# Optimization experiments

Hardware: AMD Instinct MI355X
Metric: run time of the kernel (lower is better)

The kernel has to match this reference:

```python
import jax, jax.numpy as jnp
import numpy as np

N = 100000
E = 1600000
D = 128  # in_dim == hidden_dim


def _glorot(key, shape):
    lim = np.sqrt(6.0 / (shape[0] + shape[1]))
    return jax.random.uniform(key, shape, jnp.float32, -lim, lim)


def setup_inputs() -> dict:
    key = jax.random.key(0)
    ks = jax.random.split(key, 10)
    x = jax.random.normal(ks[0], (N, D), jnp.float32)
    edge_index = jax.random.randint(ks[1], (2, E), 0, N, jnp.int64)
    return {
        "x": x,
        "edge_index": edge_index,
        "W1": _glorot(ks[2], (D, D)), "b1": jnp.zeros((D,), jnp.float32),
        "W2": _glorot(ks[3], (D, D)), "b2": jnp.zeros((D,), jnp.float32),
        "Wv": _glorot(ks[4], (D, D)), "bv": jnp.zeros((D,), jnp.float32),
        "Wt": _glorot(ks[5], (D, D)), "bt": jnp.zeros((D,), jnp.float32),
    }


def _gcn_conv(x, W, b, src, dst, dis):
    """GCNConv: x' = D^-1/2 (A+I) D^-1/2 (x W) + b (symmetric norm, self-loops)."""
    xw = x @ W  # [N, H]
    coef = dis[src] * dis[dst]  # [E]
    msg = xw[src] * coef[:, None]  # [E, H] gathered messages
    agg = jax.ops.segment_sum(msg, dst, num_segments=x.shape[0])
    agg = agg + (dis * dis)[:, None] * xw  # self-loop contribution
    return agg + b


def reference(x, edge_index, W1, b1, W2, b2, Wv, bv, Wt, bt):
    src, dst = edge_index[0], edge_index[1]
    n = x.shape[0]
    # degree including self-loop; rsqrt normalization
    deg = jax.ops.segment_sum(jnp.ones_like(dst, dtype=x.dtype), dst, num_segments=n) + 1.0
    dis = jax.lax.rsqrt(deg)
    h = jax.nn.relu(_gcn_conv(x, W1, b1, src, dst, dis))  # dropout: eval no-op
    h = _gcn_conv(h, W2, b2, src, dst, dis)  # last layer: no relu
    x_vision = jax.nn.relu(h @ Wv + bv)
    x_text = jax.nn.relu(h @ Wt + bt)
    return (h, x_vision, x_text)
```

## Files before the change

### kernel.cpp

```cpp
#include <hip/hip_runtime.h>
#include <hip/hip_bf16.h>
#include <hip/hip_fp16.h>

#define NODES 100000
#define EDGES 1600000
#define DIM   128
#define NB    782
#define KA    4096

typedef __bf16   bf16x8 __attribute__((ext_vector_type(8)));
typedef float    f32x4  __attribute__((ext_vector_type(4)));
typedef _Float16 f16x8  __attribute__((ext_vector_type(8)));

__device__ __forceinline__ void gather16(const void* gp, void* lp) {
    __builtin_amdgcn_global_load_lds(
        (const __attribute__((address_space(1))) void*)gp,
        (__attribute__((address_space(3))) void*)lp, 16, 0, 0);
}

__device__ __forceinline__ int wave_detect_m64(const void* ei) {
    const unsigned int* u = (const unsigned int*)ei;
    const unsigned long long nz = __ballot(u[2 * (threadIdx.x & 63) + 1] != 0);
    return (nz == 0ULL) ? 1 : 0;
}

__device__ __forceinline__ int load_idx(const void* ei, long long pos, int m64) {
    return m64 ? (int)((const long long*)ei)[pos] : ((const int*)ei)[pos];
}

__global__ __launch_bounds__(256) void init_kernel(
    int* __restrict__ deg, int zcnt4, int zb,
    const float* __restrict__ Wa, const float* __restrict__ Wb,
    const float* __restrict__ Wc, const float* __restrict__ Wd,
    __bf16* __restrict__ wfout)
{
    const int bid = blockIdx.x;
    if (bid < zb) {
        const int i4 = bid * 256 + threadIdx.x;
        if (i4 < zcnt4) ((int4*)deg)[i4] = make_int4(0, 0, 0, 0);
    } else {
        const int pb = bid - zb;
        const int m  = pb >> 6;
        const int d  = (pb & 63) * 256 + threadIdx.x;
        const float* W = (m == 0) ? Wa : (m == 1) ? Wb : (m == 2) ? Wc : Wd;
        const int j  = d & 7;
        const int l  = (d >> 3) & 15;
        const int q  = (d >> 7) & 3;
        const int kt = (d >> 9) & 3;
        const int ct = (d >> 11) & 7;
        wfout[m * 16384 + d] = (__bf16)W[(kt * 32 + q * 8 + j) * DIM + ct * 16 + l];
    }
}

template <int RELU_BIAS, int ABF16, int OUTF16>
__device__ __forceinline__ void gemm_body(
    const void* __restrict__ Ain, const __bf16* __restrict__ Wf,
    const float* __restrict__ bias, void* __restrict__ outp, int M, int bid)
{
    const int wave = threadIdx.x >> 6;
    const int lane = threadIdx.x & 63;
    const int l15  = lane & 15;
    const int quad = lane >> 4;

    const int row0 = bid * 128 + wave * 32;
    if (row0 >= M) return;

    bf16x8 afA[4], afB[4];
#pragma unroll
    for (int t = 0; t < 2; t++) {
        const int arow  = row0 + t * 16 + l15;
        const int arowc = arow < M ? arow : (M - 1);
        bf16x8* af = t ? afB : afA;
        if (ABF16) {
            const __bf16* ap = (const __bf16*)Ain + (size_t)arowc * DIM + quad * 8;
#pragma unroll
            for (int kt = 0; kt < 4; kt++) af[kt] = *(const bf16x8*)(ap + kt * 32);
        } else {
            const float* ap = (const float*)Ain + (size_t)arowc * DIM + quad * 8;
#pragma unroll
            for (int kt = 0; kt < 4; kt++) {
                const f32x4 lo = *(const f32x4*)(ap + kt * 32);
                const f32x4 hi = *(const f32x4*)(ap + kt * 32 + 4);
                bf16x8 r;
#pragma unroll
                for (int j = 0; j < 4; j++) { r[j] = (__bf16)lo[j]; r[j + 4] = (__bf16)hi[j]; }
                af[kt] = r;
            }
        }
    }

#pragma unroll
    for (int ct = 0; ct < 8; ct++) {
        f32x4 cA = {0.f, 0.f, 0.f, 0.f};
        f32x4 cB = {0.f, 0.f, 0.f, 0.f};
#pragma unroll
        for (int kt = 0; kt < 4; kt++) {
            const bf16x8 b = *(const bf16x8*)(Wf + (ct * 4 + kt) * 512 + lane * 8);
            cA = __builtin_amdgcn_mfma_f32_16x16x32_bf16(afA[kt], b, cA, 0, 0, 0);
            cB = __builtin_amdgcn_mfma_f32_16x16x32_bf16(afB[kt], b, cB, 0, 0, 0);
        }
        const float bb = RELU_BIAS ? bias[ct * 16 + l15] : 0.f;
#pragma unroll
        for (int t = 0; t < 2; t++) {
            const f32x4 c = t ? cB : cA;
#pragma unroll
            for (int r = 0; r < 4; r++) {
                const int row = row0 + t * 16 + quad * 4 + r;
                if (row < M) {
                    float v = c[r];
                    if (RELU_BIAS) { v += bb; v = v > 0.f ? v : 0.f; }
                    const size_t idx = (size_t)row * DIM + ct * 16 + l15;
                    if (OUTF16) ((_Float16*)outp)[idx] = (_Float16)v;
                    else        ((float*)outp)[idx]    = v;
                }
            }
        }
    }
}

template <int RELU_BIAS, int ABF16, int OUTF16>
__global__ __launch_bounds__(256) void gemm128_kernel(
    const void* __restrict__ Ain, const __bf16* __restrict__ Wf,
    const float* __restrict__ bias, void* __restrict__ outp, int M)
{
    gemm_body<RELU_BIAS, ABF16, OUTF16>(Ain, Wf, bias, outp, M, blockIdx.x);
}

__global__ __launch_bounds__(256) void gemm1_count_kernel(
    const float* __restrict__ x, const __bf16* __restrict__ wf1,
    _Float16* __restrict__ xwh, int M, int gm,
    const void* __restrict__ ei, int* __restrict__ deg, int e_cnt)
{
    const int bid = blockIdx.x;
    if (bid < gm) {
        gemm_body<0, 0, 1>(x, wf1, nullptr, xwh, M, bid);
    } else {
        const int m64 = wave_detect_m64(ei);
        const int i = (bid - gm) * 256 + threadIdx.x;
        if (i < e_cnt)
            atomicAdd(&deg[load_idx(ei, (long long)EDGES + i, m64)], 1);
    }
}

__global__ __launch_bounds__(256) void gemm128_dual_kernel(
    const float* __restrict__ A,
    const __bf16* __restrict__ Wf1, const float* __restrict__ b1,
    const __bf16* __restrict__ Wf2, const float* __restrict__ b2,
    float* __restrict__ out1, float* __restrict__ out2, int M)
{
    const int wave = threadIdx.x >> 6;
    const int lane = threadIdx.x & 63;
    const int l15  = lane & 15;
    const int quad = lane >> 4;

    const int row0 = blockIdx.x * 128 + wave * 32;
    if (row0 >= M) return;

    bf16x8 afA[4], afB[4];
#pragma unroll
    for (int t = 0; t < 2; t++) {
        const int arow  = row0 + t * 16 + l15;
        const int arowc = arow < M ? arow : (M - 1);
        const float* ap = A + (size_t)arowc * DIM + quad * 8;
        bf16x8* af = t ? afB : afA;
#pragma unroll
        for (int kt = 0; kt < 4; kt++) {
            const f32x4 lo = *(const f32x4*)(ap + kt * 32);
            const f32x4 hi = *(const f32x4*)(ap + kt * 32 + 4);
            bf16x8 r;
#pragma unroll
            for (int j = 0; j < 4; j++) { r[j] = (__bf16)lo[j]; r[j + 4] = (__bf16)hi[j]; }
            af[kt] = r;
        }
    }

#pragma unroll
    for (int ct = 0; ct < 8; ct++) {
        f32x4 cA1 = {0.f,0.f,0.f,0.f}, cA2 = {0.f,0.f,0.f,0.f};
        f32x4 cB1 = {0.f,0.f,0.f,0.f}, cB2 = {0.f,0.f,0.f,0.f};
#pragma unroll
        for (int kt = 0; kt < 4; kt++) {
            const bf16x8 w1 = *(const bf16x8*)(Wf1 + (ct * 4 + kt) * 512 + lane * 8);
            const bf16x8 w2 = *(const bf16x8*)(Wf2 + (ct * 4 + kt) * 512 + lane * 8);
            cA1 = __builtin_amdgcn_mfma_f32_16x16x32_bf16(afA[kt], w1, cA1, 0, 0, 0);
            cA2 = __builtin_amdgcn_mfma_f32_16x16x32_bf16(afA[kt], w2, cA2, 0, 0, 0);
            cB1 = __builtin_amdgcn_mfma_f32_16x16x32_bf16(afB[kt], w1, cB1, 0, 0, 0);
            cB2 = __builtin_amdgcn_mfma_f32_16x16x32_bf16(afB[kt], w2, cB2, 0, 0, 0);
        }
        const float bb1 = b1[ct * 16 + l15];
        const float bb2 = b2[ct * 16 + l15];
#pragma unroll
        for (int t = 0; t < 2; t++) {
            const f32x4 c1 = t ? cB1 : cA1;
            const f32x4 c2 = t ? cB2 : cA2;
#pragma unroll
            for (int r = 0; r < 4; r++) {
                const int row = row0 + t * 16 + quad * 4 + r;
                if (row < M) {
                    float v1 = c1[r] + bb1; v1 = v1 > 0.f ? v1 : 0.f;
                    float v2 = c2[r] + bb2; v2 = v2 > 0.f ? v2 : 0.f;
                    out1[(size_t)row * DIM + ct * 16 + l15] = v1;
                    out2[(size_t)row * DIM + ct * 16 + l15] = v2;
                }
            }
        }
    }
}

__global__ __launch_bounds__(256) void scan1_kernel(const int* __restrict__ deg,
                                                    int* __restrict__ offs,
                                                    int* __restrict__ bsum,
                                                    float* __restrict__ dis, int n) {
    __shared__ int sm[256];
    const int t = threadIdx.x, i = blockIdx.x * 256 + t;
    const int v = (i < n) ? deg[i] : 0;
    sm[t] = v;
    __syncthreads();
    for (int d = 1; d < 256; d <<= 1) {
        const int add = (t >= d) ? sm[t - d] : 0;
        __syncthreads();
        sm[t] += add;
        __syncthreads();
    }
    if (i < n) {
        offs[i] = sm[t] - v;
        dis[i]  = rsqrtf((float)v + 1.0f);
    }
    if (t == 255) bsum[blockIdx.x] = sm[255];
}

__global__ __launch_bounds__(256) void scan23_kernel(int* __restrict__ offs,
                                                     const int* __restrict__ bsum,
                                                     int* __restrict__ bcur, int n) {
    __shared__ int sm[256];
    const int t = threadIdx.x, bid = blockIdx.x;
    int part = 0;
    for (int j = t; j < bid; j += 256) part += bsum[j];
    sm[t] = part;
    __syncthreads();
    for (int d = 128; d > 0; d >>= 1) {
        if (t < d) sm[t] += sm[t + d];
        __syncthreads();
    }
    const int boff = sm[0];
    const int i = bid * 256 + t;
    if (i < n) {
        const int o = offs[i] + boff;
        offs[i] = o;
        if ((i & 127) == 0) bcur[i >> 7] = o;
    }
    if (bid == 0 && t == 0) offs[n] = EDGES;
}

__global__ __launch_bounds__(256) void bucketA_kernel(
    const void* __restrict__ ei, int* __restrict__ bcur,
    int2* __restrict__ stage, int e_cnt)
{
    __shared__ int2 sstage[KA];
    __shared__ int hist[NB], lofs[NB], lcur[NB], gbase[NB];
    __shared__ int sm[256];
    const int m64 = wave_detect_m64(ei);
    const int t = threadIdx.x;
    const int base = blockIdx.x * KA;
    int cnt = e_cnt - base; cnt = cnt < KA ? cnt : KA;

    for (int i = t; i < NB; i += 256) hist[i] = 0;
    __syncthreads();

    for (int j = t; j < cnt; j += 256) {
        const int d = load_idx(ei, (long long)EDGES + base + j, m64);
        atomicAdd(&hist[d >> 7], 1);
    }
    __syncthreads();

    const int i0 = t * 4;
    int h0 = (i0     < NB) ? hist[i0]     : 0;
    int h1 = (i0 + 1 < NB) ? hist[i0 + 1] : 0;
    int h2 = (i0 + 2 < NB) ? hist[i0 + 2] : 0;
    int h3 = (i0 + 3 < NB) ? hist[i0 + 3] : 0;
    const int psum = h0 + h1 + h2 + h3;
    sm[t] = psum;
    __syncthreads();
    for (int d = 1; d < 256; d <<= 1) {
        const int a = (t >= d) ? sm[t - d] : 0;
        __syncthreads();
        sm[t] += a;
        __syncthreads();
    }
    const int ex = sm[t] - psum;
    if (i0     < NB) { lofs[i0]     = ex;                lcur[i0]     = ex; }
    if (i0 + 1 < NB) { lofs[i0 + 1] = ex + h0;           lcur[i0 + 1] = ex + h0; }
    if (i0 + 2 < NB) { lofs[i0 + 2] = ex + h0 + h1;      lcur[i0 + 2] = ex + h0 + h1; }
    if (i0 + 3 < NB) { lofs[i0 + 3] = ex + h0 + h1 + h2; lcur[i0 + 3] = ex + h0 + h1 + h2; }
    __syncthreads();

    for (int i = t; i < NB; i += 256)
        if (hist[i] > 0) gbase[i] = atomicAdd(&bcur[i], hist[i]);
    __syncthreads();

    for (int j = t; j < cnt; j += 256) {
        const int s = load_idx(ei, base + j, m64);
        const int d = load_idx(ei, (long long)EDGES + base + j, m64);
        const int p = atomicAdd(&lcur[d >> 7], 1);
        sstage[p] = make_int2(s, d);
    }
    __syncthreads();

    for (int j = t; j < cnt; j += 256) {
        const int2 r = sstage[j];
        const int b = r.y >> 7;
        stage[gbase[b] + (j - lofs[b])] = r;
    }
}

__global__ __launch_bounds__(256) void bucketB_kernel(
    const int* __restrict__ offs, const float* __restrict__ dis,
    const int2* __restrict__ stage, int2* __restrict__ csr, int n)
{
    __shared__ int2 recs[3072];
    __shared__ int lcur[128];
    const int t  = threadIdx.x;
    const int v0 = blockIdx.x << 7;
    int nv = n - v0; nv = nv < 128 ? nv : 128;
    const int base = offs[v0];
    const int cnt  = offs[v0 + nv] - base;
    if (t < nv) lcur[t] = offs[v0 + t] - base;
    const int lim = cnt < 3072 ? cnt : 3072;
    for (int j = t; j < lim; j += 256) recs[j] = stage[base + j];
    __syncthreads();
    for (int j = t; j < lim; j += 256) {
        const int2 r = recs[j];
        const int pos = atomicAdd(&lcur[r.y - v0], 1);
        const float cf = dis[r.x] * dis[r.y];
        csr[base + pos] = make_int2(r.x, __float_as_int(cf));
    }
    for (int j = 3072 + t; j < cnt; j += 256) {
        const int2 r = stage[base + j];
        const int pos = atomicAdd(&lcur[r.y - v0], 1);
        const float cf = dis[r.x] * dis[r.y];
        csr[base + pos] = make_int2(r.x, __float_as_int(cf));
    }
}

template <int RELU, int WF32, int WBF16>
__global__ __launch_bounds__(256) void aggregate_kernel(
    const int* __restrict__ offs, const int2* __restrict__ csr,
    const float* __restrict__ dis, const _Float16* __restrict__ xw,
    const float* __restrict__ bias, float* __restrict__ out_f32,
    __bf16* __restrict__ out_bf, int n)
{
    __shared__ _Float16 sbuf[4][2][8 * DIM];
    const int wid  = threadIdx.x >> 6;
    const int v    = blockIdx.x * 4 + wid;
    const int lane = threadIdx.x & 63;
    const int l15  = lane & 15;
    const int seg  = lane >> 4;
    const int lmod = lane & 7;

    const int beg = offs[v];
    const int deg = offs[v + 1] - beg;
    const int nb  = (deg + 7) >> 3;
    int lim = beg + deg - 1; if (lim < 0) lim = 0;

    _Float16* bufA = &sbuf[wid][0][0];
    _Float16* bufB = &sbuf[wid][1][0];

    f32x4 a0 = {0.f,0.f,0.f,0.f}, a1 = {0.f,0.f,0.f,0.f};
    if (seg == 0) {
        const float dv = dis[v];
        const float s2 = dv * dv;
        const f16x8 xv = *(const f16x8*)(xw + (size_t)v * DIM + l15 * 8);
#pragma unroll
        for (int j = 0; j < 4; j++) {
            a0[j] += s2 * (float)xv[j];
            a1[j] += s2 * (float)xv[j + 4];
        }
    }

    int p0 = beg + lmod;            p0 = p0 < lim ? p0 : lim;
    int2 rc = csr[p0];
#pragma unroll
    for (int g = 0; g < 2; g++) {
        const int rs = __shfl(rc.x, g * 4 + seg);
        gather16(xw + (size_t)rs * DIM + l15 * 8, bufA + g * 512);
    }
    int p1 = beg + 8 + lmod;        p1 = p1 < lim ? p1 : lim;
    int2 rn1 = csr[p1];
    int p2 = beg + 16 + lmod;       p2 = p2 < lim ? p2 : lim;
    int2 rn2 = csr[p2];

    for (int b = 0; b < nb; ++b) {
        _Float16*       nbuf = (b & 1) ? bufA : bufB;
        const _Float16* cbuf = (b & 1) ? bufB : bufA;
        const bool more = (b + 1 < nb);
        int2 rn3 = rn2;

        if (more) {
#pragma unroll
            for (int g = 0; g < 2; g++) {
                const int rs = __shfl(rn1.x, g * 4 + seg);
                gather16(xw + (size_t)rs * DIM + l15 * 8, nbuf + g * 512);
            }
            __builtin_amdgcn_sched_barrier(0);
            int p3 = beg + (b + 3) * 8 + lmod;  p3 = p3 < lim ? p3 : lim;
            rn3 = csr[p3];
            __builtin_amdgcn_sched_barrier(0);
            asm volatile("s_waitcnt vmcnt(3)" ::: "memory");
            __builtin_amdgcn_sched_barrier(0);
        } else {
            asm volatile("s_waitcnt vmcnt(0)" ::: "memory");
            __builtin_amdgcn_sched_barrier(0);
        }

        const float cfy = __int_as_float(rc.y);
        const int rem = deg - b * 8;
#pragma unroll
        for (int s = 0; s < 2; s++) {
            const int r = s * 4 + seg;
            const float cr = __shfl(cfy, r);
            if (r < rem) {
                const f16x8 hv = *(const f16x8*)(cbuf + s * 512 + lane * 8);
#pragma unroll
                for (int j = 0; j < 4; j++) {
                    a0[j] += cr * (float)hv[j];
                    a1[j] += cr * (float)hv[j + 4];
                }
            }
        }
        rc = rn1; rn1 = rn2; rn2 = rn3;
    }

#pragma unroll
    for (int j = 0; j < 4; j++) {
        a0[j] += __shfl_xor(a0[j], 16); a0[j] += __shfl_xor(a0[j], 32);
        a1[j] += __shfl_xor(a1[j], 16); a1[j] += __shfl_xor(a1[j], 32);
    }

    if (seg == 0) {
        const int cc = l15 * 8;
#pragma unroll
        for (int j = 0; j < 4; j++) { a0[j] += bias[cc + j]; a1[j] += bias[cc + 4 + j]; }
        if (RELU) {
#pragma unroll
            for (int j = 0; j < 4; j++) {
                a0[j] = a0[j] > 0.f ? a0[j] : 0.f;
                a1[j] = a1[j] > 0.f ? a1[j] : 0.f;
            }
        }
        if (WF32) {
            *(f32x4*)(out_f32 + (size_t)v * DIM + cc)     = a0;
            *(f32x4*)(out_f32 + (size_t)v * DIM + cc + 4) = a1;
        }
        if (WBF16) {
            bf16x8 bv;
#pragma unroll
            for (int j = 0; j < 4; j++) { bv[j] = (__bf16)a0[j]; bv[j + 4] = (__bf16)a1[j]; }
            *(bf16x8*)(out_bf + (size_t)v * DIM + cc) = bv;
        }
    }
    asm volatile("s_waitcnt vmcnt(0)" ::: "memory");
}

extern "C" void kernel_launch(void* const* d_in, const int* in_sizes, int n_in,
                              void* d_out, int out_size, void* d_ws, size_t ws_size,
                              hipStream_t stream)
{
    const int N = NODES, E = EDGES;
    const size_t ND = (size_t)N * DIM;

    const float* x  = (const float*)d_in[0];
    const void*  ei = d_in[1];
    const float* W1 = (const float*)d_in[2];
    const float* b1 = (const float*)d_in[3];
    const float* W2 = (const float*)d_in[4];
    const float* b2 = (const float*)d_in[5];
    const float* Wv = (const float*)d_in[6];
    const float* bv = (const float*)d_in[7];
    const float* Wt = (const float*)d_in[8];
    const float* bt = (const float*)d_in[9];

    char* w = (char*)d_ws;
    float*  dis  = (float*)(w + 4096);
    int*    offs = (int*)(w + 524288);
    int*    bsum = (int*)(w + 1048576);
    int*    bcur = (int*)(w + 1056768);
    int*    deg  = (int*)(w + 1064960);
    int2*   csr  = (int2*)(w + 1507328);
    __bf16* wf   = (__bf16*)(w + 14311424);
    __bf16* wf1 = wf, *wf2 = wf + 16384, *wfv = wf + 32768, *wft = wf + 49152;

    float* out   = (float*)d_out;
    float* slot0 = out;
    float* slot1 = out + ND;
    float* slot2 = out + 2 * ND;
    __bf16*   h1bf  = (__bf16*)slot1;
    _Float16* xwh   = (_Float16*)slot2;
    int2*     stage = (int2*)slot0;

    const int GN   = (N + 255) / 256;
    const int GE   = (E + 255) / 256;
    const int GM   = (N + 127) / 128;
    const int GAG  = (N + 3) / 4;
    const int GA   = (E + KA - 1) / KA;
    const int GB   = NB;

    const int zcnt4 = N / 4;
    const int ZB    = (zcnt4 + 255) / 256;

    init_kernel<<<ZB + 256, 256, 0, stream>>>(deg, zcnt4, ZB, W1, W2, Wv, Wt, wf);
    gemm1_count_kernel<<<GM + GE, 256, 0, stream>>>(x, wf1, xwh, N, GM, ei, deg, E);
    scan1_kernel<<<GN, 256, 0, stream>>>(deg, offs, bsum, dis, N);
    scan23_kernel<<<GN, 256, 0, stream>>>(offs, bsum, bcur, N);
    bucketA_kernel<<<GA, 256, 0, stream>>>(ei, bcur, stage, E);
    bucketB_kernel<<<GB, 256, 0, stream>>>(offs, dis, stage, csr, N);

    aggregate_kernel<1, 0, 1><<<GAG, 256, 0, stream>>>(offs, csr, dis, xwh, b1,
                                                       nullptr, h1bf, N);
    gemm128_kernel<0, 1, 1><<<GM, 256, 0, stream>>>(h1bf, wf2, nullptr, xwh, N);
    aggregate_kernel<0, 1, 0><<<GAG, 256, 0, stream>>>(offs, csr, dis, xwh, b2,
                                                       slot0, nullptr, N);
    gemm128_dual_kernel<<<GM, 256, 0, stream>>>(slot0, wfv, bv, wft, bt, slot1, slot2, N);
}
```

Baseline: 487.2 us.

## Bucket edges into fixed-capacity regions before degree scan, fuse with first GEMM

Bucketing of edges by destination block now happens in fixed-capacity slots per bucket, with an overflow list, so it no longer needs the degree prefix scan first. The bucketing is fused into the first GEMM launch. Degrees are then counted per bucket from the staged records in a new kernel, which replaces the global atomic degree count and the deg zeroing. This reorders the CSR build pipeline so the edge list is read once up front and global atomics are avoided. In exchange it adds an overflow path that every bucket block scans, and it relies on the staging buffer (output slot0) being large enough for NB*CAP records.

Result: faster. 432.3 us (-11.3%).

```diff
diff --git a/kernel.cpp b/kernel.cpp
--- a/kernel.cpp
+++ b/kernel.cpp
@@ -7,6 +7,7 @@
 #define DIM   128
 #define NB    782
 #define KA    4096
+#define CAP   4096
 
 typedef __bf16   bf16x8 __attribute__((ext_vector_type(8)));
 typedef float    f32x4  __attribute__((ext_vector_type(4)));
@@ -29,17 +30,18 @@
 }
 
 __global__ __launch_bounds__(256) void init_kernel(
-    int* __restrict__ deg, int zcnt4, int zb,
+    int* __restrict__ bcur,
     const float* __restrict__ Wa, const float* __restrict__ Wb,
     const float* __restrict__ Wc, const float* __restrict__ Wd,
     __bf16* __restrict__ wfout)
 {
     const int bid = blockIdx.x;
-    if (bid < zb) {
-        const int i4 = bid * 256 + threadIdx.x;
-        if (i4 < zcnt4) ((int4*)deg)[i4] = make_int4(0, 0, 0, 0);
+    if (bid < 4) {
+        const int i = bid * 256 + threadIdx.x;
+        if (i < NB) bcur[i] = i * CAP;
+        if (i == NB) bcur[NB] = 0;
     } else {
-        const int pb = bid - zb;
+        const int pb = bid - 4;
         const int m  = pb >> 6;
         const int d  = (pb & 63) * 256 + threadIdx.x;
         const float* W = (m == 0) ? Wa : (m == 1) ? Wb : (m == 2) ? Wc : Wd;
@@ -126,19 +128,76 @@
     gemm_body<RELU_BIAS, ABF16, OUTF16>(Ain, Wf, bias, outp, M, blockIdx.x);
 }
 
-__global__ __launch_bounds__(256) void gemm1_count_kernel(
+__global__ __launch_bounds__(256) void gemm1_bucketA_kernel(
     const float* __restrict__ x, const __bf16* __restrict__ wf1,
     _Float16* __restrict__ xwh, int M, int gm,
-    const void* __restrict__ ei, int* __restrict__ deg, int e_cnt)
-{
+    const void* __restrict__ ei, int* __restrict__ bcur,
+    int2* __restrict__ stage, int2* __restrict__ ovf, int e_cnt)
+{
+    __shared__ int2 sstage[KA];
+    __shared__ int hist[NB], lofs[NB], lcur[NB], gbase[NB];
+    __shared__ int sm[256];
+
     const int bid = blockIdx.x;
     if (bid < gm) {
         gemm_body<0, 0, 1>(x, wf1, nullptr, xwh, M, bid);
-    } else {
-        const int m64 = wave_detect_m64(ei);
-        const int i = (bid - gm) * 256 + threadIdx.x;
-        if (i < e_cnt)
-            atomicAdd(&deg[load_idx(ei, (long long)EDGES + i, m64)], 1);
+        return;
+    }
+
+    const int m64 = wave_detect_m64(ei);
+    const int t = threadIdx.x;
+    const int base = (bid - gm) * KA;
+    int cnt = e_cnt - base; cnt = cnt < KA ? cnt : KA;
+    if (cnt <= 0) return;
+
+    for (int i = t; i < NB; i += 256) hist[i] = 0;
+    __syncthreads();
+
+    for (int j = t; j < cnt; j += 256) {
+        const int d = load_idx(ei, (long long)EDGES + base + j, m64);
+        atomicAdd(&hist[d >> 7], 1);
+    }
+    __syncthreads();
+
+    const int i0 = t * 4;
+    int h0 = (i0     < NB) ? hist[i0]     : 0;
+    int h1 = (i0 + 1 < NB) ? hist[i0 + 1] : 0;
+    int h2 = (i0 + 2 < NB) ? hist[i0 + 2] : 0;
+    int h3 = (i0 + 3 < NB) ? hist[i0 + 3] : 0;
+    const int psum = h0 + h1 + h2 + h3;
+    sm[t] = psum;
+    __syncthreads();
+    for (int d = 1; d < 256; d <<= 1) {
+        const int a = (t >= d) ? sm[t - d] : 0;
+        __syncthreads();
+        sm[t] += a;
+        __syncthreads();
+    }
+    const int ex = sm[t] - psum;
+    if (i0     < NB) { lofs[i0]     = ex;                lcur[i0]     = ex; }
+    if (i0 + 1 < NB) { lofs[i0 + 1] = ex + h0;           lcur[i0 + 1] = ex + h0; }
+    if (i0 + 2 < NB) { lofs[i0 + 2] = ex + h0 + h1;      lcur[i0 + 2] = ex + h0 + h1; }
+    if (i0 + 3 < NB) { lofs[i0 + 3] = ex + h0 + h1 + h2; lcur[i0 + 3] = ex + h0 + h1 + h2; }
+    __syncthreads();
+
+    for (int i = t; i < NB; i += 256)
+        if (hist[i] > 0) gbase[i] = atomicAdd(&bcur[i], hist[i]);
+    __syncthreads();
+
+    for (int j = t; j < cnt; j += 256) {
+        const int s = load_idx(ei, base + j, m64);
+        const int d = load_idx(ei, (long long)EDGES + base + j, m64);
+        const int p = atomicAdd(&lcur[d >> 7], 1);
+        sstage[p] = make_int2(s, d);
+    }
+    __syncthreads();
+
+    for (int j = t; j < cnt; j += 256) {
+        const int2 r = sstage[j];
+        const int b = r.y >> 7;
+        const int p = gbase[b] + (j - lofs[b]);
+        if (p < (b + 1) * CAP) stage[p] = r;
+        else                   ovf[atomicAdd(&bcur[NB], 1)] = r;
     }
 }
 
@@ -207,6 +266,28 @@
     }
 }
 
+__global__ __launch_bounds__(256) void bucketB1_kernel(
+    const int* __restrict__ bcur, const int2* __restrict__ ovf,
+    const int2* __restrict__ stage, int* __restrict__ deg, int n)
+{
+    __shared__ int ldeg[128];
+    const int t = threadIdx.x, b = blockIdx.x;
+    const int v0 = b << 7;
+    if (t < 128) ldeg[t] = 0;
+    __syncthreads();
+    int cnt = bcur[b] - b * CAP; cnt = cnt < CAP ? cnt : CAP;
+    const int2* reg = stage + (size_t)b * CAP;
+    for (int j = t; j < cnt; j += 256) atomicAdd(&ldeg[reg[j].y & 127], 1);
+    const int no = bcur[NB];
+    for (int j = t; j < no; j += 256) {
+        const int2 r = ovf[j];
+        if ((r.y >> 7) == b) atomicAdd(&ldeg[r.y & 127], 1);
+    }
+    __syncthreads();
+    const int v = v0 + t;
+    if (t < 128 && v < n) deg[v] = ldeg[t];
+}
+
 __global__ __launch_bounds__(256) void scan1_kernel(const int* __restrict__ deg,
                                                     int* __restrict__ offs,
                                                     int* __restrict__ bsum,
@@ -230,8 +311,7 @@
 }
 
 __global__ __launch_bounds__(256) void scan23_kernel(int* __restrict__ offs,
-                                                     const int* __restrict__ bsum,
-                                                     int* __restrict__ bcur, int n) {
+                                                     const int* __restrict__ bsum, int n) {
     __shared__ int sm[256];
     const int t = threadIdx.x, bid = blockIdx.x;
     int part = 0;
@@ -244,101 +324,35 @@
     }
     const int boff = sm[0];
     const int i = bid * 256 + t;
-    if (i < n) {
-        const int o = offs[i] + boff;
-        offs[i] = o;
-        if ((i & 127) == 0) bcur[i >> 7] = o;
-    }
+    if (i < n) offs[i] += boff;
     if (bid == 0 && t == 0) offs[n] = EDGES;
 }
 
-__global__ __launch_bounds__(256) void bucketA_kernel(
-    const void* __restrict__ ei, int* __restrict__ bcur,
-    int2* __restrict__ stage, int e_cnt)
-{
-    __shared__ int2 sstage[KA];
-    __shared__ int hist[NB], lofs[NB], lcur[NB], gbase[NB];
-    __shared__ int sm[256];
-    const int m64 = wave_detect_m64(ei);
-    const int t = threadIdx.x;
-    const int base = blockIdx.x * KA;
-    int cnt = e_cnt - base; cnt = cnt < KA ? cnt : KA;
-
-    for (int i = t; i < NB; i += 256) hist[i] = 0;
-    __syncthreads();
-
+__global__ __launch_bounds__(256) void bucketB2_kernel(
+    const int* __restrict__ offs, const float* __restrict__ dis,
+    const int* __restrict__ bcur, const int2* __restrict__ ovf,
+    const int2* __restrict__ stage, int2* __restrict__ csr, int n)
+{
+    __shared__ int lcur[128];
+    const int t = threadIdx.x, b = blockIdx.x;
+    const int v0 = b << 7;
+    int nv = n - v0; nv = nv < 128 ? nv : 128;
+    if (t < nv) lcur[t] = offs[v0 + t];
+    __syncthreads();
+    int cnt = bcur[b] - b * CAP; cnt = cnt < CAP ? cnt : CAP;
+    const int2* reg = stage + (size_t)b * CAP;
     for (int j = t; j < cnt; j += 256) {
-        const int d = load_idx(ei, (long long)EDGES + base + j, m64);
-        atomicAdd(&hist[d >> 7], 1);
-    }
-    __syncthreads();
-
-    const int i0 = t * 4;
-    int h0 = (i0     < NB) ? hist[i0]     : 0;
-    int h1 = (i0 + 1 < NB) ? hist[i0 + 1] : 0;
-    int h2 = (i0 + 2 < NB) ? hist[i0 + 2] : 0;
-    int h3 = (i0 + 3 < NB) ? hist[i0 + 3] : 0;
-    const int psum = h0 + h1 + h2 + h3;
-    sm[t] = psum;
-    __syncthreads();
-    for (int d = 1; d < 256; d <<= 1) {
-        const int a = (t >= d) ? sm[t - d] : 0;
-        __syncthreads();
-        sm[t] += a;
-        __syncthreads();
-    }
-    const int ex = sm[t] - psum;
-    if (i0     < NB) { lofs[i0]     = ex;                lcur[i0]     = ex; }
-    if (i0 + 1 < NB) { lofs[i0 + 1] = ex + h0;           lcur[i0 + 1] = ex + h0; }
-    if (i0 + 2 < NB) { lofs[i0 + 2] = ex + h0 + h1;      lcur[i0 + 2] = ex + h0 + h1; }
-    if (i0 + 3 < NB) { lofs[i0 + 3] = ex + h0 + h1 + h2; lcur[i0 + 3] = ex + h0 + h1 + h2; }
-    __syncthreads();
-
-    for (int i = t; i < NB; i += 256)
-        if (hist[i] > 0) gbase[i] = atomicAdd(&bcur[i], hist[i]);
-    __syncthreads();
-
-    for (int j = t; j < cnt; j += 256) {
-        const int s = load_idx(ei, base + j, m64);
-        const int d = load_idx(ei, (long long)EDGES + base + j, m64);
-        const int p = atomicAdd(&lcur[d >> 7], 1);
-        sstage[p] = make_int2(s, d);
-    }
-    __syncthreads();
-
-    for (int j = t; j < cnt; j += 256) {
-        const int2 r = sstage[j];
-        const int b = r.y >> 7;
-        stage[gbase[b] + (j - lofs[b])] = r;
-    }
-}
-
-__global__ __launch_bounds__(256) void bucketB_kernel(
-    const int* __restrict__ offs, const float* __restrict__ dis,
-    const int2* __restrict__ stage, int2* __restrict__ csr, int n)
-{
-    __shared__ int2 recs[3072];
-    __shared__ int lcur[128];
-    const int t  = threadIdx.x;
-    const int v0 = blockIdx.x << 7;
-    int nv = n - v0; nv = nv < 128 ? nv : 128;
-    const int base = offs[v0];
-    const int cnt  = offs[v0 + nv] - base;
-    if (t < nv) lcur[t] = offs[v0 + t] - base;
-    const int lim = cnt < 3072 ? cnt : 3072;
-    for (int j = t; j < lim; j += 256) recs[j] = stage[base + j];
-    __syncthreads();
-    for (int j = t; j < lim; j += 256) {
-        const int2 r = recs[j];
-        const int pos = atomicAdd(&lcur[r.y - v0], 1);
-        const float cf = dis[r.x] * dis[r.y];
-        csr[base + pos] = make_int2(r.x, __float_as_int(cf));
-    }
-    for (int j = 3072 + t; j < cnt; j += 256) {
-        const int2 r = stage[base + j];
-        const int pos = atomicAdd(&lcur[r.y - v0], 1);
-        const float cf = dis[r.x] * dis[r.y];
-        csr[base + pos] = make_int2(r.x, __float_as_int(cf));
+        const int2 r = reg[j];
+        const int pos = atomicAdd(&lcur[r.y & 127], 1);
+        csr[pos] = make_int2(r.x, __float_as_int(dis[r.x] * dis[r.y]));
+    }
+    const int no = bcur[NB];
+    for (int j = t; j < no; j += 256) {
+        const int2 r = ovf[j];
+        if ((r.y >> 7) == b) {
+            const int pos = atomicAdd(&lcur[r.y & 127], 1);
+            csr[pos] = make_int2(r.x, __float_as_int(dis[r.x] * dis[r.y]));
+        }
     }
 }
 
@@ -496,23 +510,21 @@
     __bf16*   h1bf  = (__bf16*)slot1;
     _Float16* xwh   = (_Float16*)slot2;
     int2*     stage = (int2*)slot0;
+    int2*     ovf   = (int2*)slot1;
 
     const int GN   = (N + 255) / 256;
-    const int GE   = (E + 255) / 256;
     const int GM   = (N + 127) / 128;
     const int GAG  = (N + 3) / 4;
     const int GA   = (E + KA - 1) / KA;
     const int GB   = NB;
 
-    const int zcnt4 = N / 4;
-    const int ZB    = (zcnt4 + 255) / 256;
-
-    init_kernel<<<ZB + 256, 256, 0, stream>>>(deg, zcnt4, ZB, W1, W2, Wv, Wt, wf);
-    gemm1_count_kernel<<<GM + GE, 256, 0, stream>>>(x, wf1, xwh, N, GM, ei, deg, E);
+    init_kernel<<<4 + 256, 256, 0, stream>>>(bcur, W1, W2, Wv, Wt, wf);
+    gemm1_bucketA_kernel<<<GM + GA, 256, 0, stream>>>(x, wf1, xwh, N, GM,
+                                                      ei, bcur, stage, ovf, E);
+    bucketB1_kernel<<<GB, 256, 0, stream>>>(bcur, ovf, stage, deg, N);
     scan1_kernel<<<GN, 256, 0, stream>>>(deg, offs, bsum, dis, N);
-    scan23_kernel<<<GN, 256, 0, stream>>>(offs, bsum, bcur, N);
-    bucketA_kernel<<<GA, 256, 0, stream>>>(ei, bcur, stage, E);
-    bucketB_kernel<<<GB, 256, 0, stream>>>(offs, dis, stage, csr, N);
+    scan23_kernel<<<GN, 256, 0, stream>>>(offs, bsum, N);
+    bucketB2_kernel<<<GB, 256, 0, stream>>>(offs, dis, bcur, ovf, stage, csr, N);
 
     aggregate_kernel<1, 0, 1><<<GAG, 256, 0, stream>>>(offs, csr, dis, xwh, b1,
                                                        nullptr, h1bf, N);
```
